# Kernel tuning notes

Measured on AMD Instinct MI355X. Metric: run time of the kernel, lower is better.

The kernel has to match this reference:

```python
import jax, jax.numpy as jnp
import numpy as np

SHARED_DIM = 512
ENC_IN = 512
LATENT = 16
BATCH = 65536
NUM_CLASSES = 16


def setup_inputs() -> dict:
    key = jax.random.key(0)
    ks = jax.random.split(key, 12)
    s = 1.0 / np.sqrt(SHARED_DIM)
    si = 1.0 / np.sqrt(ENC_IN)
    return {
        "x": jax.random.normal(ks[0], (BATCH, ENC_IN), dtype=jnp.float32),
        # shared MLP: two ReLU hiddens + identity output (rlkit Mlp)
        "W0": jax.random.uniform(ks[1], (SHARED_DIM, ENC_IN), jnp.float32, -si, si),
        "b0": jnp.zeros((SHARED_DIM,), jnp.float32),
        "W1": jax.random.uniform(ks[2], (SHARED_DIM, SHARED_DIM), jnp.float32, -s, s),
        "b1": jnp.zeros((SHARED_DIM,), jnp.float32),
        "W2": jax.random.uniform(ks[3], (SHARED_DIM, SHARED_DIM), jnp.float32, -s, s),
        "b2": jnp.zeros((SHARED_DIM,), jnp.float32),
        # class encoder (router)
        "Wc": jax.random.uniform(ks[4], (NUM_CLASSES, SHARED_DIM), jnp.float32, -s, s),
        "bc": jnp.zeros((NUM_CLASSES,), jnp.float32),
        # per-class gaussian experts, stacked: [K, 2*latent, shared_dim]
        "Wg": jax.random.uniform(ks[5], (NUM_CLASSES, 2 * LATENT, SHARED_DIM), jnp.float32, -s, s),
        "bg": jnp.zeros((NUM_CLASSES, 2 * LATENT), jnp.float32),
    }


def reference(x, W0, b0, W1, b1, W2, b2, Wc, bc, Wg, bg):
    # shared encoder: ReLU MLP with identity output layer
    m = jax.nn.relu(x @ W0.T + b0)
    m = jax.nn.relu(m @ W1.T + b1)
    m = m @ W2.T + b2                      # [B, D]
    # router: softmax over classes, then most-likely class per sample
    y_probs = jax.nn.softmax(m @ Wc.T + bc, axis=-1)   # [B, K]
    y = jnp.argmax(y_probs, axis=1)                    # [B]
    # evaluate ALL per-class experts densely (as the original does)
    mu_sigma = jnp.einsum('bd,ked->bke', m, Wg) + bg   # [B, K, 2L]
    mu = mu_sigma[..., :LATENT]                        # Normal mean; sampler='mean'
    # gather the selected class's mean per sample
    z = jnp.take_along_axis(mu, y[:, None, None], axis=1)[:, 0, :]  # [B, L]
    return (z, y)
```

## Files before the change

### kernel.cpp

```cpp
#include <hip/hip_runtime.h>
#include <hip/hip_bf16.h>

typedef __attribute__((ext_vector_type(8))) short short8;
typedef __attribute__((ext_vector_type(16))) float floatx16;
typedef __attribute__((ext_vector_type(4))) float floatx4;

#define AS1 __attribute__((address_space(1)))
#define AS3 __attribute__((address_space(3)))

constexpr int MM = 65536;
constexpr int KK = 512;
constexpr int NN = 512;

#define GM 128
#define GN 128
#define GK 32
#define LDT 40

__device__ __forceinline__ unsigned short bf16_rn(float v) {
  unsigned u = __float_as_uint(v);
  return (unsigned short)((u + 0x7FFFu + ((u >> 16) & 1u)) >> 16);
}
__device__ __forceinline__ float bf16_to_f32(unsigned short h) {
  return __uint_as_float((unsigned)h << 16);
}

__global__ __launch_bounds__(256) void split_kernel(
    const float* __restrict__ src, unsigned short* __restrict__ h,
    unsigned short* __restrict__ l, int n4) {
  int i = blockIdx.x * 256 + threadIdx.x;
  if (i >= n4) return;
  float4 v = ((const float4*)src)[i];
  ushort4 hv, lv;
  hv.x = bf16_rn(v.x); lv.x = bf16_rn(v.x - bf16_to_f32(hv.x));
  hv.y = bf16_rn(v.y); lv.y = bf16_rn(v.y - bf16_to_f32(hv.y));
  hv.z = bf16_rn(v.z); lv.z = bf16_rn(v.z - bf16_to_f32(hv.z));
  hv.w = bf16_rn(v.w); lv.w = bf16_rn(v.w - bf16_to_f32(hv.w));
  ((ushort4*)h)[i] = hv;
  ((ushort4*)l)[i] = lv;
}

template<bool RELU, bool SPLIT>
__global__ __launch_bounds__(256, 2) void gemm_mfma(
    const unsigned short* __restrict__ Ah, const unsigned short* __restrict__ Al,
    const unsigned short* __restrict__ Wh, const unsigned short* __restrict__ Wl,
    const float* __restrict__ bias,
    unsigned short* __restrict__ Ch, unsigned short* __restrict__ Cl,
    float* __restrict__ Cf) {
  __shared__ __align__(16) unsigned short sAh[2][GM][GK], sAl[2][GM][GK];
  __shared__ __align__(16) unsigned short sBh[2][GN][GK], sBl[2][GN][GK];
  const int tid = threadIdx.x;
  const int lane = tid & 63;
  const int wid = tid >> 6;
  const int wr = wid >> 1;
  const int wc = wid & 1;
  const int bm = blockIdx.x, bn = blockIdx.y;
  const size_t Abase = (size_t)bm * GM * KK;
  const size_t Bbase = (size_t)bn * GN * KK;

  const unsigned short* gsrc; unsigned short* ldst; size_t tb;
  if (wid == 0)      { gsrc = Ah; tb = Abase; ldst = &sAh[0][0][0]; }
  else if (wid == 1) { gsrc = Al; tb = Abase; ldst = &sAl[0][0][0]; }
  else if (wid == 2) { gsrc = Wh; tb = Bbase; ldst = &sBh[0][0][0]; }
  else               { gsrc = Wl; tb = Bbase; ldst = &sBl[0][0][0]; }
  const int rowl = lane >> 2;
  const int gch  = (lane & 3) ^ ((lane >> 3) & 3);
  const unsigned short* gbase = gsrc + tb + (size_t)rowl * KK + gch * 8;

  auto stage = [&](int buf, int kk) {
#pragma unroll
    for (int j = 0; j < 8; ++j) {
      __builtin_amdgcn_global_load_lds(
          (const AS1 unsigned int*)(gbase + (size_t)(j * 16) * KK + kk),
          (AS3 unsigned int*)(ldst + buf * (GM * GK) + j * 16 * GK),
          16, 0, 0);
    }
  };

  floatx16 acc[2][2];
#pragma unroll
  for (int i = 0; i < 2; ++i)
#pragma unroll
    for (int j = 0; j < 2; ++j)
#pragma unroll
      for (int r = 0; r < 16; ++r) acc[i][j][r] = 0.f;

  stage(0, 0);
  __syncthreads();

  const int swz = (lane >> 1) & 3;
  int cur = 0;
  for (int k0 = 0; k0 < KK; k0 += GK) {
    if (k0 + GK < KK) stage(cur ^ 1, k0 + GK);

    const unsigned short* pAh = &sAh[cur][0][0];
    const unsigned short* pAl = &sAl[cur][0][0];
    const unsigned short* pBh = &sBh[cur][0][0];
    const unsigned short* pBl = &sBl[cur][0][0];
#pragma unroll
    for (int ks = 0; ks < 2; ++ks) {
      const int ch = ks * 2 + (lane >> 5);
      const int sw = (ch ^ swz) * 8;
      short8 fah[2], fal[2], fbh[2], fbl[2];
#pragma unroll
      for (int ri = 0; ri < 2; ++ri) {
        int row = wr * 64 + ri * 32 + (lane & 31);
        fah[ri] = *(const short8*)(pAh + row * GK + sw);
        fal[ri] = *(const short8*)(pAl + row * GK + sw);
      }
#pragma unroll
      for (int si = 0; si < 2; ++si) {
        int col = wc * 64 + si * 32 + (lane & 31);
        fbh[si] = *(const short8*)(pBh + col * GK + sw);
        fbl[si] = *(const short8*)(pBl + col * GK + sw);
      }
#pragma unroll
      for (int ri = 0; ri < 2; ++ri)
#pragma unroll
        for (int si = 0; si < 2; ++si) {
          acc[ri][si] = __builtin_amdgcn_mfma_f32_32x32x16_bf16(fah[ri], fbh[si], acc[ri][si], 0, 0, 0);
          acc[ri][si] = __builtin_amdgcn_mfma_f32_32x32x16_bf16(fah[ri], fbl[si], acc[ri][si], 0, 0, 0);
          acc[ri][si] = __builtin_amdgcn_mfma_f32_32x32x16_bf16(fal[ri], fbh[si], acc[ri][si], 0, 0, 0);
        }
    }
    __syncthreads();
    cur ^= 1;
  }

#pragma unroll
  for (int si = 0; si < 2; ++si) {
    int col = bn * GN + wc * 64 + si * 32 + (lane & 31);
    float bv = bias[col];
#pragma unroll
    for (int ri = 0; ri < 2; ++ri) {
#pragma unroll
      for (int r = 0; r < 16; ++r) {
        int row = bm * GM + wr * 64 + ri * 32 + (r & 3) + 8 * (r >> 2) + 4 * (lane >> 5);
        float v = acc[ri][si][r] + bv;
        if (RELU) v = fmaxf(v, 0.f);
        size_t idx = (size_t)row * NN + col;
        if (SPLIT) {
          unsigned short h = bf16_rn(v);
          Ch[idx] = h;
          Cl[idx] = bf16_rn(v - bf16_to_f32(h));
        } else {
          Cf[idx] = v;
        }
      }
    }
  }
}

__global__ __launch_bounds__(256, 2) void gemm_muz(
    const unsigned short* __restrict__ Ahm, const unsigned short* __restrict__ Wh,
    const float* __restrict__ bias, const float* __restrict__ y_in,
    float* __restrict__ z_out) {
  __shared__ __align__(16) unsigned short sAh[2][GM][GK];
  __shared__ __align__(16) unsigned short sBh[2][GN][GK];
  const int tid = threadIdx.x;
  const int lane = tid & 63;
  const int wid = tid >> 6;
  const int wr = wid >> 1;
  const int wc = wid & 1;
  const int bm = blockIdx.x, bn = blockIdx.y;
  const size_t Abase = (size_t)bm * GM * KK;
  const size_t Bbase = (size_t)bn * GN * KK;

  const unsigned short* gsrc = (wid < 2) ? Ahm : Wh;
  const size_t tb = (wid < 2) ? Abase : Bbase;
  unsigned short* ldst = (wid < 2) ? &sAh[0][0][0] : &sBh[0][0][0];
  const int rbase = (wid & 1) * 64;
  const int rowl = lane >> 2;
  const int gch  = (lane & 3) ^ ((lane >> 3) & 3);
  const unsigned short* gbase = gsrc + tb + (size_t)rowl * KK + gch * 8;

  auto stage = [&](int buf, int kk) {
#pragma unroll
    for (int j = 0; j < 4; ++j) {
      const int r0 = rbase + j * 16;
      __builtin_amdgcn_global_load_lds(
          (const AS1 unsigned int*)(gbase + (size_t)r0 * KK + kk),
          (AS3 unsigned int*)(ldst + buf * (GM * GK) + r0 * GK),
          16, 0, 0);
    }
  };

  floatx16 acc[2][2];
#pragma unroll
  for (int i = 0; i < 2; ++i)
#pragma unroll
    for (int j = 0; j < 2; ++j)
#pragma unroll
      for (int r = 0; r < 16; ++r) acc[i][j][r] = 0.f;

  stage(0, 0);
  __syncthreads();

  const int swz = (lane >> 1) & 3;
  int cur = 0;
  for (int k0 = 0; k0 < KK; k0 += GK) {
    if (k0 + GK < KK) stage(cur ^ 1, k0 + GK);
    const unsigned short* pA = &sAh[cur][0][0];
    const unsigned short* pB = &sBh[cur][0][0];
#pragma unroll
    for (int ks = 0; ks < 2; ++ks) {
      const int ch = ks * 2 + (lane >> 5);
      const int sw = (ch ^ swz) * 8;
      short8 fa[2], fb[2];
#pragma unroll
      for (int ri = 0; ri < 2; ++ri) {
        int row = wr * 64 + ri * 32 + (lane & 31);
        fa[ri] = *(const short8*)(pA + row * GK + sw);
      }
#pragma unroll
      for (int si = 0; si < 2; ++si) {
        int col = wc * 64 + si * 32 + (lane & 31);
        fb[si] = *(const short8*)(pB + col * GK + sw);
      }
#pragma unroll
      for (int ri = 0; ri < 2; ++ri)
#pragma unroll
        for (int si = 0; si < 2; ++si)
          acc[ri][si] = __builtin_amdgcn_mfma_f32_32x32x16_bf16(fa[ri], fb[si], acc[ri][si], 0, 0, 0);
    }
    __syncthreads();
    cur ^= 1;
  }

  int colv[2]; float bv[2];
#pragma unroll
  for (int si = 0; si < 2; ++si) {
    colv[si] = bn * GN + wc * 64 + si * 32 + (lane & 31);
    bv[si] = bias[colv[si]];
  }
#pragma unroll
  for (int ri = 0; ri < 2; ++ri)
#pragma unroll
    for (int r = 0; r < 16; ++r) {
      int row = bm * GM + wr * 64 + ri * 32 + (r & 3) + 8 * (r >> 2) + 4 * (lane >> 5);
      int yv = (int)y_in[row];
#pragma unroll
      for (int si = 0; si < 2; ++si) {
        if ((colv[si] >> 4) == yv)
          z_out[(size_t)row * 16 + (colv[si] & 15)] = acc[ri][si][r] + bv[si];
      }
    }
}

__global__ __launch_bounds__(256) void logits_kernel(
    const unsigned short* __restrict__ mh, const unsigned short* __restrict__ ml,
    const unsigned short* __restrict__ wch, const unsigned short* __restrict__ wcl,
    const float* __restrict__ bc, float* __restrict__ y_out) {
  __shared__ unsigned short smh[64][LDT], sml[64][LDT];
  __shared__ float slog[64][17];
  const int tid = threadIdx.x;
  const int lane = tid & 63;
  const int wid = tid >> 6;
  const size_t row0 = (size_t)blockIdx.x * 64;
  const int fr = lane & 15;
  const int fq = lane >> 4;

  floatx4 acc = {0.f, 0.f, 0.f, 0.f};
  const unsigned short* bh = wch + fr * 512 + fq * 8;
  const unsigned short* bl = wcl + fr * 512 + fq * 8;

  for (int k0 = 0; k0 < 512; k0 += 32) {
    {
      int row = tid >> 2, cc = (tid & 3) * 8;
      size_t g = (row0 + row) * 512 + k0 + cc;
      *(short8*)&smh[row][cc] = *(const short8*)(mh + g);
      *(short8*)&sml[row][cc] = *(const short8*)(ml + g);
    }
    __syncthreads();
    short8 ah = *(const short8*)&smh[wid * 16 + fr][fq * 8];
    short8 al = *(const short8*)&sml[wid * 16 + fr][fq * 8];
    short8 fbh = *(const short8*)(bh + k0);
    short8 fbl = *(const short8*)(bl + k0);
    acc = __builtin_amdgcn_mfma_f32_16x16x32_bf16(ah, fbh, acc, 0, 0, 0);
    acc = __builtin_amdgcn_mfma_f32_16x16x32_bf16(ah, fbl, acc, 0, 0, 0);
    acc = __builtin_amdgcn_mfma_f32_16x16x32_bf16(al, fbh, acc, 0, 0, 0);
    __syncthreads();
  }
#pragma unroll
  for (int r = 0; r < 4; ++r)
    slog[wid * 16 + fq * 4 + r][fr] = acc[r] + bc[fr];
  __syncthreads();
  if (tid < 64) {
    float best = slog[tid][0];
    int bi = 0;
#pragma unroll
    for (int j = 1; j < 16; ++j) {
      float v = slog[tid][j];
      if (v > best) { best = v; bi = j; }
    }
    y_out[row0 + tid] = (float)bi;
  }
}

__global__ __launch_bounds__(256) void prep_wg(
    const float* __restrict__ Wg, const float* __restrict__ bg,
    unsigned short* __restrict__ wgh, float* __restrict__ wgb) {
  int gid = blockIdx.x * 256 + threadIdx.x;
  if (gid >= 32768) return;
  int r = gid >> 7;
  int c4 = (gid & 127) * 4;
  int k = r >> 4, e = r & 15;
  float4 v = *(const float4*)(Wg + ((size_t)k * 32 + e) * 512 + c4);
  ushort4 h;
  h.x = bf16_rn(v.x); h.y = bf16_rn(v.y); h.z = bf16_rn(v.z); h.w = bf16_rn(v.w);
  *(ushort4*)(wgh + (size_t)r * 512 + c4) = h;
  if (c4 == 0) wgb[r] = bg[k * 32 + e];
}

extern "C" void kernel_launch(void* const* d_in, const int* in_sizes, int n_in,
                              void* d_out, int out_size, void* d_ws, size_t ws_size,
                              hipStream_t stream) {
  const float* x  = (const float*)d_in[0];
  const float* W0 = (const float*)d_in[1];
  const float* b0 = (const float*)d_in[2];
  const float* W1 = (const float*)d_in[3];
  const float* b1 = (const float*)d_in[4];
  const float* W2 = (const float*)d_in[5];
  const float* b2 = (const float*)d_in[6];
  const float* Wc = (const float*)d_in[7];
  const float* bc = (const float*)d_in[8];
  const float* Wg = (const float*)d_in[9];
  const float* bg = (const float*)d_in[10];

  const size_t NEL = (size_t)MM * KK;
  unsigned short* Ah = (unsigned short*)d_ws;
  unsigned short* Al = Ah + NEL;
  unsigned short* Bh = Al + NEL;
  unsigned short* Bl = Bh + NEL;
  unsigned short* wch = Al;
  unsigned short* wcl = Al + 8192;
  unsigned short* wgh = Al + 16384;
  float* wgb = (float*)(Al + 16384 + 131072);

  unsigned short* w0h = (unsigned short*)d_out;
  unsigned short* w0l = w0h + 262144;
  unsigned short* w1h = w0l + 262144;
  unsigned short* w1l = w1h + 262144;
  unsigned short* w2h = w1l + 262144;
  unsigned short* w2l = w2h + 262144;

  float* z_out = (float*)d_out;
  float* y_out = z_out + (size_t)MM * 16;

  split_kernel<<<(int)(NEL / 4 / 256), 256, 0, stream>>>(x, Ah, Al, (int)(NEL / 4));
  split_kernel<<<256, 256, 0, stream>>>(W0, w0h, w0l, 65536);
  split_kernel<<<256, 256, 0, stream>>>(W1, w1h, w1l, 65536);
  split_kernel<<<256, 256, 0, stream>>>(W2, w2h, w2l, 65536);

  dim3 grid(MM / GM, NN / GN);
  gemm_mfma<true , true ><<<grid, 256, 0, stream>>>(Ah, Al, w0h, w0l, b0, Bh, Bl, nullptr);
  gemm_mfma<true , true ><<<grid, 256, 0, stream>>>(Bh, Bl, w1h, w1l, b1, Ah, Al, nullptr);
  gemm_mfma<false, true ><<<grid, 256, 0, stream>>>(Ah, Al, w2h, w2l, b2, Bh, Bl, nullptr);

  split_kernel<<<8, 256, 0, stream>>>(Wc, wch, wcl, 2048);
  prep_wg<<<128, 256, 0, stream>>>(Wg, bg, wgh, wgb);

  logits_kernel<<<MM / 64, 256, 0, stream>>>(Bh, Bl, wch, wcl, bc, y_out);
  gemm_muz<<<dim3(MM / GM, 2), 256, 0, stream>>>(Bh, wgh, wgb, y_out, z_out);
}
```

Before: 681.4 us.

## Overlap next-tile loads via partial vmcnt waits and stage split epilogue through LDS

Replaces the full __syncthreads in the K loop with a partial vmcnt wait plus raw s_barrier. The wait lets the next tile's global-to-LDS loads stay in flight while the current tile is consumed, instead of draining all memory ops each iteration. In the split GEMM, the epilogue now packs the hi/lo bf16 outputs into LDS and writes them back as coalesced ushort4 rows, replacing scattered 2-byte stores. It relies on correct hand-tuned vmcnt counts and unrolls the K loop fully, which adds code size and register pressure.

Measured after the change: 688.7 us. About the same (+1.1%).

```diff
diff --git a/kernel.cpp b/kernel.cpp
--- a/kernel.cpp
+++ b/kernel.cpp
@@ -47,8 +47,11 @@
     const float* __restrict__ bias,
     unsigned short* __restrict__ Ch, unsigned short* __restrict__ Cl,
     float* __restrict__ Cf) {
-  __shared__ __align__(16) unsigned short sAh[2][GM][GK], sAl[2][GM][GK];
-  __shared__ __align__(16) unsigned short sBh[2][GN][GK], sBl[2][GN][GK];
+  __shared__ __align__(16) unsigned short smem[32768];
+  unsigned short* sAh = smem;
+  unsigned short* sAl = smem + 8192;
+  unsigned short* sBh = smem + 16384;
+  unsigned short* sBl = smem + 24576;
   const int tid = threadIdx.x;
   const int lane = tid & 63;
   const int wid = tid >> 6;
@@ -59,10 +62,10 @@
   const size_t Bbase = (size_t)bn * GN * KK;
 
   const unsigned short* gsrc; unsigned short* ldst; size_t tb;
-  if (wid == 0)      { gsrc = Ah; tb = Abase; ldst = &sAh[0][0][0]; }
-  else if (wid == 1) { gsrc = Al; tb = Abase; ldst = &sAl[0][0][0]; }
-  else if (wid == 2) { gsrc = Wh; tb = Bbase; ldst = &sBh[0][0][0]; }
-  else               { gsrc = Wl; tb = Bbase; ldst = &sBl[0][0][0]; }
+  if (wid == 0)      { gsrc = Ah; tb = Abase; ldst = sAh; }
+  else if (wid == 1) { gsrc = Al; tb = Abase; ldst = sAl; }
+  else if (wid == 2) { gsrc = Wh; tb = Bbase; ldst = sBh; }
+  else               { gsrc = Wl; tb = Bbase; ldst = sBl; }
   const int rowl = lane >> 2;
   const int gch  = (lane & 3) ^ ((lane >> 3) & 3);
   const unsigned short* gbase = gsrc + tb + (size_t)rowl * KK + gch * 8;
@@ -72,7 +75,7 @@
     for (int j = 0; j < 8; ++j) {
       __builtin_amdgcn_global_load_lds(
           (const AS1 unsigned int*)(gbase + (size_t)(j * 16) * KK + kk),
-          (AS3 unsigned int*)(ldst + buf * (GM * GK) + j * 16 * GK),
+          (AS3 unsigned int*)(ldst + buf * 4096 + j * 16 * GK),
           16, 0, 0);
     }
   };
@@ -86,17 +89,24 @@
       for (int r = 0; r < 16; ++r) acc[i][j][r] = 0.f;
 
   stage(0, 0);
-  __syncthreads();
 
   const int swz = (lane >> 1) & 3;
   int cur = 0;
+#pragma unroll
   for (int k0 = 0; k0 < KK; k0 += GK) {
-    if (k0 + GK < KK) stage(cur ^ 1, k0 + GK);
-
-    const unsigned short* pAh = &sAh[cur][0][0];
-    const unsigned short* pAl = &sAl[cur][0][0];
-    const unsigned short* pBh = &sBh[cur][0][0];
-    const unsigned short* pBl = &sBl[cur][0][0];
+    if (k0 + GK < KK) {
+      stage(cur ^ 1, k0 + GK);
+      asm volatile("s_waitcnt vmcnt(8)" ::: "memory");
+    } else {
+      asm volatile("s_waitcnt vmcnt(0)" ::: "memory");
+    }
+    __builtin_amdgcn_s_barrier();
+    __builtin_amdgcn_sched_barrier(0);
+
+    const unsigned short* pAh = sAh + cur * 4096;
+    const unsigned short* pAl = sAl + cur * 4096;
+    const unsigned short* pBh = sBh + cur * 4096;
+    const unsigned short* pBl = sBl + cur * 4096;
 #pragma unroll
     for (int ks = 0; ks < 2; ++ks) {
       const int ch = ks * 2 + (lane >> 5);
@@ -123,28 +133,59 @@
           acc[ri][si] = __builtin_amdgcn_mfma_f32_32x32x16_bf16(fal[ri], fbh[si], acc[ri][si], 0, 0, 0);
         }
     }
+    __builtin_amdgcn_sched_barrier(0);
+    __builtin_amdgcn_s_barrier();
+    cur ^= 1;
+  }
+
+  if (SPLIT) {
+    unsigned* lds32 = (unsigned*)smem;
+#pragma unroll
+    for (int si = 0; si < 2; ++si) {
+      int colL = wc * 64 + si * 32 + (lane & 31);
+      float bv = bias[bn * GN + colL];
+#pragma unroll
+      for (int ri = 0; ri < 2; ++ri) {
+#pragma unroll
+        for (int r = 0; r < 16; ++r) {
+          int rowL = wr * 64 + ri * 32 + (r & 3) + 8 * (r >> 2) + 4 * (lane >> 5);
+          float v = acc[ri][si][r] + bv;
+          if (RELU) v = fmaxf(v, 0.f);
+          unsigned short h = bf16_rn(v);
+          unsigned short lo = bf16_rn(v - bf16_to_f32(h));
+          lds32[rowL * 128 + colL] = (unsigned)h | ((unsigned)lo << 16);
+        }
+      }
+    }
     __syncthreads();
-    cur ^= 1;
-  }
-
-#pragma unroll
-  for (int si = 0; si < 2; ++si) {
-    int col = bn * GN + wc * 64 + si * 32 + (lane & 31);
-    float bv = bias[col];
-#pragma unroll
-    for (int ri = 0; ri < 2; ++ri) {
-#pragma unroll
-      for (int r = 0; r < 16; ++r) {
-        int row = bm * GM + wr * 64 + ri * 32 + (r & 3) + 8 * (r >> 2) + 4 * (lane >> 5);
-        float v = acc[ri][si][r] + bv;
-        if (RELU) v = fmaxf(v, 0.f);
-        size_t idx = (size_t)row * NN + col;
-        if (SPLIT) {
-          unsigned short h = bf16_rn(v);
-          Ch[idx] = h;
-          Cl[idx] = bf16_rn(v - bf16_to_f32(h));
-        } else {
-          Cf[idx] = v;
+    const int rrow = tid >> 5;
+    const int rcol4 = (tid & 31) * 4;
+#pragma unroll
+    for (int p = 0; p < 16; ++p) {
+      int row = p * 8 + rrow;
+      uint4 d = *(const uint4*)&lds32[row * 128 + rcol4];
+      ushort4 hv, lv;
+      hv.x = (unsigned short)(d.x); lv.x = (unsigned short)(d.x >> 16);
+      hv.y = (unsigned short)(d.y); lv.y = (unsigned short)(d.y >> 16);
+      hv.z = (unsigned short)(d.z); lv.z = (unsigned short)(d.z >> 16);
+      hv.w = (unsigned short)(d.w); lv.w = (unsigned short)(d.w >> 16);
+      size_t gi = (size_t)(bm * GM + row) * NN + bn * GN + rcol4;
+      *(ushort4*)&Ch[gi] = hv;
+      *(ushort4*)&Cl[gi] = lv;
+    }
+  } else {
+#pragma unroll
+    for (int si = 0; si < 2; ++si) {
+      int col = bn * GN + wc * 64 + si * 32 + (lane & 31);
+      float bv = bias[col];
+#pragma unroll
+      for (int ri = 0; ri < 2; ++ri) {
+#pragma unroll
+        for (int r = 0; r < 16; ++r) {
+          int row = bm * GM + wr * 64 + ri * 32 + (r & 3) + 8 * (r >> 2) + 4 * (lane >> 5);
+          float v = acc[ri][si][r] + bv;
+          if (RELU) v = fmaxf(v, 0.f);
+          Cf[(size_t)row * NN + col] = v;
         }
       }
     }
@@ -155,8 +196,9 @@
     const unsigned short* __restrict__ Ahm, const unsigned short* __restrict__ Wh,
     const float* __restrict__ bias, const float* __restrict__ y_in,
     float* __restrict__ z_out) {
-  __shared__ __align__(16) unsigned short sAh[2][GM][GK];
-  __shared__ __align__(16) unsigned short sBh[2][GN][GK];
+  __shared__ __align__(16) unsigned short smem[16384];
+  unsigned short* sA = smem;
+  unsigned short* sB = smem + 8192;
   const int tid = threadIdx.x;
   const int lane = tid & 63;
   const int wid = tid >> 6;
@@ -168,7 +210,7 @@
 
   const unsigned short* gsrc = (wid < 2) ? Ahm : Wh;
   const size_t tb = (wid < 2) ? Abase : Bbase;
-  unsigned short* ldst = (wid < 2) ? &sAh[0][0][0] : &sBh[0][0][0];
+  unsigned short* ldst = (wid < 2) ? sA : sB;
   const int rbase = (wid & 1) * 64;
   const int rowl = lane >> 2;
   const int gch  = (lane & 3) ^ ((lane >> 3) & 3);
@@ -180,7 +222,7 @@
       const int r0 = rbase + j * 16;
       __builtin_amdgcn_global_load_lds(
           (const AS1 unsigned int*)(gbase + (size_t)r0 * KK + kk),
-          (AS3 unsigned int*)(ldst + buf * (GM * GK) + r0 * GK),
+          (AS3 unsigned int*)(ldst + buf * 4096 + r0 * GK),
           16, 0, 0);
     }
   };
@@ -194,14 +236,22 @@
       for (int r = 0; r < 16; ++r) acc[i][j][r] = 0.f;
 
   stage(0, 0);
-  __syncthreads();
 
   const int swz = (lane >> 1) & 3;
   int cur = 0;
+#pragma unroll
   for (int k0 = 0; k0 < KK; k0 += GK) {
-    if (k0 + GK < KK) stage(cur ^ 1, k0 + GK);
-    const unsigned short* pA = &sAh[cur][0][0];
-    const unsigned short* pB = &sBh[cur][0][0];
+    if (k0 + GK < KK) {
+      stage(cur ^ 1, k0 + GK);
+      asm volatile("s_waitcnt vmcnt(4)" ::: "memory");
+    } else {
+      asm volatile("s_waitcnt vmcnt(0)" ::: "memory");
+    }
+    __builtin_amdgcn_s_barrier();
+    __builtin_amdgcn_sched_barrier(0);
+
+    const unsigned short* pA = sA + cur * 4096;
+    const unsigned short* pB = sB + cur * 4096;
 #pragma unroll
     for (int ks = 0; ks < 2; ++ks) {
       const int ch = ks * 2 + (lane >> 5);
@@ -223,7 +273,8 @@
         for (int si = 0; si < 2; ++si)
           acc[ri][si] = __builtin_amdgcn_mfma_f32_32x32x16_bf16(fa[ri], fb[si], acc[ri][si], 0, 0, 0);
     }
-    __syncthreads();
+    __builtin_amdgcn_sched_barrier(0);
+    __builtin_amdgcn_s_barrier();
     cur ^= 1;
   }
 
```
